# Kernel tuning notes

Hardware: AMD Instinct MI355X
Metric: run time of the kernel (lower is better)

## Reference

```python
import jax, jax.numpy as jnp
import numpy as np

E = 768
H_HEADS = 12


def trilinear_border_sample(feat_map, coords):
    """grid_sample 3D, mode='bilinear', padding_mode='border', align_corners=True.
    feat_map: (B, C, D, H, W); coords: (B, P, 3) in [-1,1], last dim = (x, y, z) -> (W, H, D).
    Returns (B, P, C).
    """
    B, C, D, H, W = feat_map.shape
    x, y, z = coords[..., 0], coords[..., 1], coords[..., 2]
    ix = (x + 1.0) * 0.5 * (W - 1)
    iy = (y + 1.0) * 0.5 * (H - 1)
    iz = (z + 1.0) * 0.5 * (D - 1)
    x0 = jnp.floor(ix); y0 = jnp.floor(iy); z0 = jnp.floor(iz)
    wx = ix - x0; wy = iy - y0; wz = iz - z0
    x0i = jnp.clip(x0, 0, W - 1).astype(jnp.int32)
    x1i = jnp.clip(x0 + 1, 0, W - 1).astype(jnp.int32)
    y0i = jnp.clip(y0, 0, H - 1).astype(jnp.int32)
    y1i = jnp.clip(y0 + 1, 0, H - 1).astype(jnp.int32)
    z0i = jnp.clip(z0, 0, D - 1).astype(jnp.int32)
    z1i = jnp.clip(z0 + 1, 0, D - 1).astype(jnp.int32)
    flat = feat_map.reshape(B, C, D * H * W)

    def gather(zi, yi, xi):
        idx = (zi * H + yi) * W + xi  # (B, P)
        return jnp.take_along_axis(flat, idx[:, None, :], axis=2)  # (B, C, P)

    out = (
        gather(z0i, y0i, x0i) * ((1 - wz) * (1 - wy) * (1 - wx))[:, None, :]
        + gather(z0i, y0i, x1i) * ((1 - wz) * (1 - wy) * wx)[:, None, :]
        + gather(z0i, y1i, x0i) * ((1 - wz) * wy * (1 - wx))[:, None, :]
        + gather(z0i, y1i, x1i) * ((1 - wz) * wy * wx)[:, None, :]
        + gather(z1i, y0i, x0i) * (wz * (1 - wy) * (1 - wx))[:, None, :]
        + gather(z1i, y0i, x1i) * (wz * (1 - wy) * wx)[:, None, :]
        + gather(z1i, y1i, x0i) * (wz * wy * (1 - wx))[:, None, :]
        + gather(z1i, y1i, x1i) * (wz * wy * wx)[:, None, :]
    )
    return out.transpose(0, 2, 1)  # (B, P, C)


def setup_inputs() -> dict:
    key = jax.random.key(0)
    ks = jax.random.split(key, 12)
    B, fullN, nb = 64, 513, 32
    s = 1.0 / np.sqrt(E)
    return {
        "x": jax.random.normal(ks[0], (B, fullN, E), jnp.float32),
        "bio_embed": jax.random.normal(ks[1], (B, E), jnp.float32),
        "base_coords": jax.random.uniform(ks[2], (nb, 3), jnp.float32),
        "offsets": jax.random.normal(ks[3], (B, nb, 3), jnp.float32) * 0.1,
        "confidence": jax.random.uniform(ks[4], (B, 1), jnp.float32),
        "sample_proj_w": jax.random.uniform(ks[5], (E, E), jnp.float32, -s, s),
        "sample_proj_b": jax.random.uniform(ks[6], (E,), jnp.float32, -s, s),
        "in_proj_w": jax.random.uniform(ks[7], (3 * E, E), jnp.float32, -s, s),
        "in_proj_b": jnp.zeros((3 * E,), jnp.float32),
        "out_proj_w": jax.random.uniform(ks[8], (E, E), jnp.float32, -s, s),
        "out_proj_b": jnp.zeros((E,), jnp.float32),
        "grid_size": 8,
    }


def reference(x, bio_embed, base_coords, offsets, confidence,
              sample_proj_w, sample_proj_b, in_proj_w, in_proj_b,
              out_proj_w, out_proj_b, grid_size):
    B, fullN, C = x.shape
    G = grid_size
    patch_tokens = x[:, 1:, :]  # (B, N, C), N = G^3
    feat_map = patch_tokens.transpose(0, 2, 1).reshape(B, C, G, G, G)

    coords = jnp.clip(base_coords[None, :, :] + offsets, -1.0, 1.0)  # (B, nb, 3)
    sampled = trilinear_border_sample(feat_map, coords)  # (B, nb, C)
    sampled = sampled @ sample_proj_w.T + sample_proj_b

    # MultiheadAttention: single query (bio_embed), keys/values = sampled tokens
    hd = E // H_HEADS
    Wq, Wk, Wv = in_proj_w[:E], in_proj_w[E:2 * E], in_proj_w[2 * E:]
    bq, bk, bv = in_proj_b[:E], in_proj_b[E:2 * E], in_proj_b[2 * E:]
    q = (bio_embed @ Wq.T + bq).reshape(B, H_HEADS, hd)
    k = (sampled @ Wk.T + bk).reshape(B, -1, H_HEADS, hd)
    v = (sampled @ Wv.T + bv).reshape(B, -1, H_HEADS, hd)
    scores = jnp.einsum('bhd,bphd->bhp', q, k) / jnp.sqrt(jnp.asarray(hd, q.dtype))
    attn = jax.nn.softmax(scores, axis=-1)
    ctx = jnp.einsum('bhp,bphd->bhd', attn, v).reshape(B, E)
    attn_out = ctx @ out_proj_w.T + out_proj_b  # (B, E)

    out = jnp.broadcast_to(attn_out[:, None, :], (B, fullN, C))
    out = out * confidence[:, :, None]
    return out
```

## Files before the change

### kernel.cpp

```cpp
#include <hip/hip_runtime.h>
#include <hip/hip_bf16.h>
#include <math.h>

#define E 768
#define NH 12
#define HD 64
#define NTHR 256
#define SLICES 8

typedef __attribute__((ext_vector_type(8))) short bf16x8;
typedef __attribute__((ext_vector_type(4))) float f32x4;

__device__ __forceinline__ unsigned short f2bf_rne(float f) {
    unsigned int u = __float_as_uint(f);
    u += 0x7FFF + ((u >> 16) & 1);
    return (unsigned short)(u >> 16);
}

__device__ __forceinline__ void sample_one(
    const float* x, const float* bcrd, const float* offs, int G,
    unsigned short* sampled, int u, int P, int fullN, int t, int tstep)
{
    int b = u / P, p = u % P;
    float gm1 = (float)(G - 1);

    float cx = bcrd[p * 3 + 0] + offs[u * 3 + 0];
    float cy = bcrd[p * 3 + 1] + offs[u * 3 + 1];
    float cz = bcrd[p * 3 + 2] + offs[u * 3 + 2];
    cx = fminf(fmaxf(cx, -1.f), 1.f);
    cy = fminf(fmaxf(cy, -1.f), 1.f);
    cz = fminf(fmaxf(cz, -1.f), 1.f);

    float ix = (cx + 1.f) * 0.5f * gm1;
    float iy = (cy + 1.f) * 0.5f * gm1;
    float iz = (cz + 1.f) * 0.5f * gm1;
    float fx = floorf(ix), fy = floorf(iy), fz = floorf(iz);
    float wx = ix - fx, wy = iy - fy, wz = iz - fz;

    int x0 = (int)fminf(fmaxf(fx,       0.f), gm1);
    int x1 = (int)fminf(fmaxf(fx + 1.f, 0.f), gm1);
    int y0 = (int)fminf(fmaxf(fy,       0.f), gm1);
    int y1 = (int)fminf(fmaxf(fy + 1.f, 0.f), gm1);
    int z0 = (int)fminf(fmaxf(fz,       0.f), gm1);
    int z1 = (int)fminf(fmaxf(fz + 1.f, 0.f), gm1);

    int tk[8];
    tk[0] = (z0 * G + y0) * G + x0;
    tk[1] = (z0 * G + y0) * G + x1;
    tk[2] = (z0 * G + y1) * G + x0;
    tk[3] = (z0 * G + y1) * G + x1;
    tk[4] = (z1 * G + y0) * G + x0;
    tk[5] = (z1 * G + y0) * G + x1;
    tk[6] = (z1 * G + y1) * G + x0;
    tk[7] = (z1 * G + y1) * G + x1;
    float wgt[8];
    wgt[0] = (1.f - wz) * (1.f - wy) * (1.f - wx);
    wgt[1] = (1.f - wz) * (1.f - wy) * wx;
    wgt[2] = (1.f - wz) * wy * (1.f - wx);
    wgt[3] = (1.f - wz) * wy * wx;
    wgt[4] = wz * (1.f - wy) * (1.f - wx);
    wgt[5] = wz * (1.f - wy) * wx;
    wgt[6] = wz * wy * (1.f - wx);
    wgt[7] = wz * wy * wx;

    const float4* xb4 = (const float4*)(x + ((size_t)b * fullN + 1) * E);
    ushort4* outp = (ushort4*)(sampled + (size_t)u * E);
    for (int c4 = t; c4 < E / 4; c4 += tstep) {
        float4 acc = {0.f, 0.f, 0.f, 0.f};
#pragma unroll
        for (int k = 0; k < 8; ++k) {
            float4 v = xb4[(size_t)tk[k] * (E / 4) + c4];
            acc.x += wgt[k] * v.x; acc.y += wgt[k] * v.y;
            acc.z += wgt[k] * v.z; acc.w += wgt[k] * v.w;
        }
        ushort4 o;
        o.x = f2bf_rne(acc.x); o.y = f2bf_rne(acc.y);
        o.z = f2bf_rne(acc.z); o.w = f2bf_rne(acc.w);
        outp[c4] = o;
    }
}

__device__ __forceinline__ void gemm64_tile(
    const unsigned short* A, const unsigned short* W,
    const float* bias, float* C,
    int N, int K, int m0, int n0,
    unsigned short* lsA, unsigned short* lsB)
{
    int wv = threadIdx.x >> 6;
    int ln = threadIdx.x & 63;
    int wm = (wv & 1) * 32;
    int wn = (wv >> 1) * 32;

    f32x4 acc[2][2] = {};

    int srow = ln >> 2;
    int scol = (ln & 3) * 8;

    for (int k0 = 0; k0 < K; k0 += 32) {
        int row = wv * 16 + srow;
        const unsigned short* ga = A + (size_t)(m0 + row) * K + k0 + scol;
        const unsigned short* gw = W + (size_t)(n0 + row) * K + k0 + scol;
        __builtin_amdgcn_global_load_lds(
            (const __attribute__((address_space(1))) unsigned int*)ga,
            (__attribute__((address_space(3))) unsigned int*)(lsA + wv * 16 * 32),
            16, 0, 0);
        __builtin_amdgcn_global_load_lds(
            (const __attribute__((address_space(1))) unsigned int*)gw,
            (__attribute__((address_space(3))) unsigned int*)(lsB + wv * 16 * 32),
            16, 0, 0);
        __syncthreads();

        int kq = (ln >> 4) * 8;
        int rsel = ln & 15;
        bf16x8 af[2], bfr[2];
#pragma unroll
        for (int i = 0; i < 2; ++i) {
            af[i]  = *(const bf16x8*)&lsA[(wm + i * 16 + rsel) * 32 + kq];
            bfr[i] = *(const bf16x8*)&lsB[(wn + i * 16 + rsel) * 32 + kq];
        }
#pragma unroll
        for (int i = 0; i < 2; ++i)
#pragma unroll
            for (int j = 0; j < 2; ++j)
                acc[i][j] = __builtin_amdgcn_mfma_f32_16x16x32_bf16(
                    af[i], bfr[j], acc[i][j], 0, 0, 0);
        __syncthreads();
    }

    int cr = (ln >> 4) * 4;
    int cc = ln & 15;
#pragma unroll
    for (int j = 0; j < 2; ++j) {
        int col = n0 + wn + j * 16 + cc;
        float bv = bias[col];
#pragma unroll
        for (int i = 0; i < 2; ++i) {
#pragma unroll
            for (int r = 0; r < 4; ++r) {
                int row = m0 + wm + i * 16 + cr + r;
                C[(size_t)row * N + col] = acc[i][j][r] + bv;
            }
        }
    }
}

__device__ __forceinline__ void w2_tile(
    const float* Wkv, const float* spw, unsigned short* w2_bf,
    int n0, int k0, unsigned short* lsA, unsigned short* lsB)
{
    int t = threadIdx.x;
    int wv = t >> 6;
    int ln = t & 63;
    int wm = (wv & 1) * 32;
    int wn = (wv >> 1) * 32;

    f32x4 acc[2][2] = {};

    for (int j0 = 0; j0 < E; j0 += 32) {
#pragma unroll
        for (int rep = 0; rep < 2; ++rep) {
            int fi = t + rep * 256;
            int r = fi >> 3, c4 = fi & 7;
            float4 v = *(const float4*)(Wkv + (size_t)(n0 + r) * E + j0 + c4 * 4);
            ushort4 o;
            o.x = f2bf_rne(v.x); o.y = f2bf_rne(v.y);
            o.z = f2bf_rne(v.z); o.w = f2bf_rne(v.w);
            *(ushort4*)(lsA + r * 32 + c4 * 4) = o;
        }
#pragma unroll
        for (int rep = 0; rep < 2; ++rep) {
            int fi = t + rep * 256;
            int kk = fi >> 3, j4 = fi & 7;
            const float* sp = spw + (size_t)(j0 + j4 * 4) * E + k0 + kk;
            ushort4 o;
            o.x = f2bf_rne(sp[0 * E]);
            o.y = f2bf_rne(sp[1 * E]);
            o.z = f2bf_rne(sp[2 * E]);
            o.w = f2bf_rne(sp[3 * E]);
            *(ushort4*)(lsB + kk * 32 + j4 * 4) = o;
        }
        __syncthreads();

        int kq = (ln >> 4) * 8;
        int rsel = ln & 15;
        bf16x8 af[2], bfr[2];
#pragma unroll
        for (int i = 0; i < 2; ++i) {
            af[i]  = *(const bf16x8*)&lsA[(wm + i * 16 + rsel) * 32 + kq];
            bfr[i] = *(const bf16x8*)&lsB[(wn + i * 16 + rsel) * 32 + kq];
        }
#pragma unroll
        for (int i = 0; i < 2; ++i)
#pragma unroll
            for (int j = 0; j < 2; ++j)
                acc[i][j] = __builtin_amdgcn_mfma_f32_16x16x32_bf16(
                    af[i], bfr[j], acc[i][j], 0, 0, 0);
        __syncthreads();
    }

    int cr = (ln >> 4) * 4;
    int cc = ln & 15;
#pragma unroll
    for (int j = 0; j < 2; ++j) {
        int col = k0 + wn + j * 16 + cc;
#pragma unroll
        for (int i = 0; i < 2; ++i) {
#pragma unroll
            for (int r = 0; r < 4; ++r) {
                int row = n0 + wm + i * 16 + cr + r;
                w2_bf[(size_t)row * E + col] = f2bf_rne(acc[i][j][r]);
            }
        }
    }
}

__device__ __forceinline__ void matvec_wave(
    const float* A, const float* W, const float* bias, float* C,
    int u, int N, int K, int ln)
{
    int m = u / N, n = u % N;
    const float* a = A + (size_t)m * K;
    const float* w = W + (size_t)n * K;
    float s = 0.f;
    for (int k = ln; k < K; k += 64) s += a[k] * w[k];
#pragma unroll
    for (int off = 32; off; off >>= 1) s += __shfl_down(s, off);
    if (ln == 0) C[u] = s + bias[n];
}

__device__ __forceinline__ void matvec_wave_v4(
    const float* A, const float* W, const float* bias, float* C,
    int u, int N, int ln)
{
    int m = u / N, n = u % N;
    const float4* a4 = (const float4*)(A + (size_t)m * E);
    const float4* w4 = (const float4*)(W + (size_t)n * E);
    float s = 0.f;
#pragma unroll
    for (int j = 0; j < 3; ++j) {
        float4 av = a4[ln + 64 * j];
        float4 wv = w4[ln + 64 * j];
        s += av.x * wv.x + av.y * wv.y + av.z * wv.z + av.w * wv.w;
    }
#pragma unroll
    for (int off = 32; off; off >>= 1) s += __shfl_down(s, off);
    if (ln == 0) C[u] = s + bias[n];
}

__global__ __launch_bounds__(256) void prep_kernel(
    const float* __restrict__ x,
    const float* __restrict__ bcrd, const float* __restrict__ offs,
    const int* __restrict__ gsize,
    const float* __restrict__ bio,
    const float* __restrict__ spw, const float* __restrict__ spb,
    const float* __restrict__ ipw, const float* __restrict__ ipb,
    unsigned short* __restrict__ sampled_bf, unsigned short* __restrict__ w2_bf,
    float* __restrict__ q, float* __restrict__ b2,
    int B, int P, int fullN, int nb_sample, int nb_w2, int nb_q)
{
    __shared__ unsigned short lsA[64 * 32];
    __shared__ unsigned short lsB[64 * 32];

    int blk = blockIdx.x;
    int t = threadIdx.x;
    int wv = t >> 6, ln = t & 63;
    const float* Wkv = ipw + (size_t)E * E;

    if (blk < nb_sample) {
        sample_one(x, bcrd, offs, *gsize, sampled_bf, blk, P, fullN, t, NTHR);
        return;
    }
    blk -= nb_sample;
    if (blk < nb_w2) {
        w2_tile(Wkv, spw, w2_bf, (blk / 12) * 64, (blk % 12) * 64, lsA, lsB);
        return;
    }
    blk -= nb_w2;
    if (blk < nb_q) {
        int u = blk * 4 + wv;
        if (u < B * E) matvec_wave_v4(bio, ipw, ipb, q, u, E, ln);
        return;
    }
    blk -= nb_q;
    {
        int u = blk * 4 + wv;
        if (u < 2 * E) matvec_wave_v4(spb, Wkv, ipb + E, b2, u, 2 * E, ln);
    }
}

__global__ __launch_bounds__(256) void kv_gemm(
    const unsigned short* __restrict__ A,
    const unsigned short* __restrict__ W,
    const float* __restrict__ bias,
    float* __restrict__ C, int N, int K)
{
    __shared__ unsigned short lsA[64 * 32];
    __shared__ unsigned short lsB[64 * 32];
    gemm64_tile(A, W, bias, C, N, K, blockIdx.y * 64, blockIdx.x * 64, lsA, lsB);
}

__global__ __launch_bounds__(256) void attn_outproj(
    const float* __restrict__ q, const float* __restrict__ kv,
    const float* __restrict__ opw, const float* __restrict__ opb,
    float* __restrict__ aout, int B, int P)
{
    __shared__ __align__(16) float q_lds[E];
    __shared__ __align__(16) float ctx_lds[E];

    int b = blockIdx.x % B;
    int g = blockIdx.x / B;
    int t = threadIdx.x, wv = t >> 6, ln = t & 63;

    const float* kvb = kv + (size_t)b * P * (2 * E);

    for (int i = t; i < E; i += NTHR) q_lds[i] = q[(size_t)b * E + i];
    __syncthreads();

    for (int h = wv; h < NH; h += 4) {
        int krow = (ln < P) ? ln : 0;
        const float4* kr4 = (const float4*)(kvb + (size_t)krow * (2 * E) + h * HD);
        const float* qh = q_lds + h * HD;
        float accd = 0.f;
#pragma unroll
        for (int j = 0; j < HD / 4; ++j) {
            float4 k4 = kr4[j];
            accd += qh[4 * j] * k4.x + qh[4 * j + 1] * k4.y
                  + qh[4 * j + 2] * k4.z + qh[4 * j + 3] * k4.w;
        }
        float s = (ln < P) ? accd * 0.125f : -INFINITY;

        float mx = s;
#pragma unroll
        for (int off = 32; off; off >>= 1) mx = fmaxf(mx, __shfl_xor(mx, off));
        float ex = (ln < P) ? __expf(s - mx) : 0.f;
        float den = ex;
#pragma unroll
        for (int off = 32; off; off >>= 1) den += __shfl_xor(den, off);
        float pl = ex / den;

        const float* vcol = kvb + E + h * HD + ln;
        float acc = 0.f;
#pragma unroll
        for (int p = 0; p < 32; ++p)
            acc += __shfl(pl, p) * vcol[(size_t)p * (2 * E)];
        ctx_lds[h * HD + ln] = acc;
    }
    __syncthreads();

    const float4* c4p = (const float4*)ctx_lds;
#pragma unroll 2
    for (int idx = 0; idx < 24; ++idx) {
        int n = g * 96 + wv * 24 + idx;
        const float4* w4 = (const float4*)(opw + (size_t)n * E);
        float s = 0.f;
#pragma unroll
        for (int j = 0; j < 3; ++j) {
            float4 wvv = w4[ln + 64 * j];
            float4 cv = c4p[ln + 64 * j];
            s += wvv.x * cv.x + wvv.y * cv.y + wvv.z * cv.z + wvv.w * cv.w;
        }
#pragma unroll
        for (int off = 32; off; off >>= 1) s += __shfl_down(s, off);
        if (ln == 0) aout[(size_t)b * E + n] = s + opb[n];
    }
}

__global__ void bcast_kernel(const float* __restrict__ attn_out,
                             const float* __restrict__ conf,
                             float* __restrict__ out,
                             int fullN, int pc)
{
    int b = blockIdx.y;
    float cf = conf[b];
    const float4* ao = (const float4*)(attn_out + (size_t)b * E);
    float4* ob = (float4*)(out + (size_t)b * fullN * E);
    int i = blockIdx.x * blockDim.x + threadIdx.x;
    if (i < pc) {
        int c4 = i % (E / 4);
        float4 v = ao[c4];
        v.x *= cf; v.y *= cf; v.z *= cf; v.w *= cf;
        ob[i] = v;
    }
}

__global__ void attn_fb(const float* __restrict__ q,
                        const float* __restrict__ kv,
                        float* __restrict__ ctx, int B, int P)
{
    int u = blockIdx.x * 4 + (threadIdx.x >> 6);
    int ln = threadIdx.x & 63;
    if (u >= B * NH) return;
    int b = u / NH, h = u % NH;
    float qd = q[(size_t)b * E + h * HD + ln];
    const float* kvb = kv + (size_t)b * P * (2 * E);
    int krow = (ln < P) ? ln : 0;
    const float* kr = kvb + (size_t)krow * (2 * E) + h * HD;
    float accd = 0.f;
#pragma unroll
    for (int e = 0; e < HD; ++e) accd += __shfl(qd, e) * kr[e];
    float s = (ln < P) ? accd * 0.125f : -INFINITY;
    float mx = s;
#pragma unroll
    for (int off = 32; off; off >>= 1) mx = fmaxf(mx, __shfl_xor(mx, off));
    float ex = (ln < P) ? __expf(s - mx) : 0.f;
    float den = ex;
#pragma unroll
    for (int off = 32; off; off >>= 1) den += __shfl_xor(den, off);
    float pl = ex / den;
    float acc = 0.f;
    for (int p = 0; p < P; ++p)
        acc += __shfl(pl, p) * kvb[(size_t)p * (2 * E) + E + h * HD + ln];
    ctx[(size_t)b * E + h * HD + ln] = acc;
}

__global__ void matvec_fb(const float* __restrict__ A,
                          const float* __restrict__ W,
                          const float* __restrict__ bias,
                          float* __restrict__ C, int M, int N, int K)
{
    int u = blockIdx.x * 4 + (threadIdx.x >> 6);
    if (u < M * N) matvec_wave(A, W, bias, C, u, N, K, threadIdx.x & 63);
}

extern "C" void kernel_launch(void* const* d_in, const int* in_sizes, int n_in,
                              void* d_out, int out_size, void* d_ws, size_t ws_size,
                              hipStream_t stream)
{
    const float* x      = (const float*)d_in[0];
    const float* bio    = (const float*)d_in[1];
    const float* bcrd   = (const float*)d_in[2];
    const float* offs   = (const float*)d_in[3];
    const float* conf   = (const float*)d_in[4];
    const float* spw    = (const float*)d_in[5];
    const float* spb    = (const float*)d_in[6];
    const float* ipw    = (const float*)d_in[7];
    const float* ipb    = (const float*)d_in[8];
    const float* opw    = (const float*)d_in[9];
    const float* opb    = (const float*)d_in[10];
    const int*   gsize  = (const int*)d_in[11];
    float* out = (float*)d_out;

    int B     = in_sizes[1] / E;
    int P     = in_sizes[2] / 3;
    int fullN = in_sizes[0] / (B * E);
    int M     = B * P;

    char* base = (char*)d_out;
    unsigned short* sampled_bf = (unsigned short*)(base + 0);
    unsigned short* w2_bf      = (unsigned short*)(base + 3145728);

    const size_t kv_bytes = (size_t)M * (2 * E) * 4;
    const size_t q_bytes  = (size_t)B * E * 4;
    const size_t b2_bytes = (size_t)(2 * E) * 4;
    const size_t ao_bytes = (size_t)B * E * 4;
    const bool path_a = (ws_size >= kv_bytes + q_bytes + b2_bytes + ao_bytes);

    float *kv, *q, *b2, *aout;
    if (path_a) {
        kv   = (float*)d_ws;
        q    = (float*)((char*)d_ws + kv_bytes);
        b2   = (float*)((char*)d_ws + kv_bytes + q_bytes);
        aout = (float*)((char*)d_ws + kv_bytes + q_bytes + b2_bytes);
    } else {
        kv   = (float*)(base + 5505024);
        q    = (float*)(base + 18087936);
        b2   = (float*)(base + 18481152);
        aout = (float*)d_ws;
    }

    int nb_sample = M;
    int nb_w2     = (2 * E / 64) * (E / 64);
    int nb_q      = (B * E + 3) / 4;
    int nb_b2     = (2 * E + 3) / 4;
    prep_kernel<<<nb_sample + nb_w2 + nb_q + nb_b2, NTHR, 0, stream>>>(
        x, bcrd, offs, gsize, bio, spw, spb, ipw, ipb,
        sampled_bf, w2_bf, q, b2, B, P, fullN, nb_sample, nb_w2, nb_q);

    kv_gemm<<<dim3(2 * E / 64, M / 64), NTHR, 0, stream>>>(
        sampled_bf, w2_bf, b2, kv, 2 * E, E);

    if (path_a) {
        attn_outproj<<<B * SLICES, NTHR, 0, stream>>>(q, kv, opw, opb, aout,
                                                      B, P);
    } else {
        float* ctx = (float*)(base + 18284544);
        attn_fb<<<(B * NH + 3) / 4, NTHR, 0, stream>>>(q, kv, ctx, B, P);
        matvec_fb<<<(B * E + 3) / 4, NTHR, 0, stream>>>(ctx, opw, opb, aout,
                                                        B, E, E);
    }

    int pc = fullN * E / 4;
    bcast_kernel<<<dim3((pc + 255) / 256, B), NTHR, 0, stream>>>(
        aout, conf, out, fullN, pc);
}
```

Baseline: 271.4 us.

## Replace explicit K/V GEMM with per-head query-folded attention over sampled tokens

Instead of materialising the full K and V projections for every sampled token with an MFMA GEMM, each (batch, head) block folds the query into the combined key weight (u = q·W2k). It then scores the raw bf16 sampled tokens against u, applies the attention weights to the raw tokens, and projects the resulting context through W2v once. This removes the large fp32 KV buffer write and read, and the separate GEMM launch. In exchange it adds a per-head matvec over W2 rows for each of the 768 blocks, and it drops the key bias term, which is safe only because softmax is shift-invariant. Out-projection becomes its own kernel reading ctx from workspace, and the fallback path for a small workspace is removed.

```diff
diff --git a/kernel.cpp b/kernel.cpp
--- a/kernel.cpp
+++ b/kernel.cpp
@@ -15,6 +15,10 @@
     unsigned int u = __float_as_uint(f);
     u += 0x7FFF + ((u >> 16) & 1);
     return (unsigned short)(u >> 16);
+}
+
+__device__ __forceinline__ float bf2f(unsigned short u) {
+    return __uint_as_float((unsigned)u << 16);
 }
 
 __device__ __forceinline__ void sample_one(
@@ -80,70 +84,6 @@
     }
 }
 
-__device__ __forceinline__ void gemm64_tile(
-    const unsigned short* A, const unsigned short* W,
-    const float* bias, float* C,
-    int N, int K, int m0, int n0,
-    unsigned short* lsA, unsigned short* lsB)
-{
-    int wv = threadIdx.x >> 6;
-    int ln = threadIdx.x & 63;
-    int wm = (wv & 1) * 32;
-    int wn = (wv >> 1) * 32;
-
-    f32x4 acc[2][2] = {};
-
-    int srow = ln >> 2;
-    int scol = (ln & 3) * 8;
-
-    for (int k0 = 0; k0 < K; k0 += 32) {
-        int row = wv * 16 + srow;
-        const unsigned short* ga = A + (size_t)(m0 + row) * K + k0 + scol;
-        const unsigned short* gw = W + (size_t)(n0 + row) * K + k0 + scol;
-        __builtin_amdgcn_global_load_lds(
-            (const __attribute__((address_space(1))) unsigned int*)ga,
-            (__attribute__((address_space(3))) unsigned int*)(lsA + wv * 16 * 32),
-            16, 0, 0);
-        __builtin_amdgcn_global_load_lds(
-            (const __attribute__((address_space(1))) unsigned int*)gw,
-            (__attribute__((address_space(3))) unsigned int*)(lsB + wv * 16 * 32),
-            16, 0, 0);
-        __syncthreads();
-
-        int kq = (ln >> 4) * 8;
-        int rsel = ln & 15;
-        bf16x8 af[2], bfr[2];
-#pragma unroll
-        for (int i = 0; i < 2; ++i) {
-            af[i]  = *(const bf16x8*)&lsA[(wm + i * 16 + rsel) * 32 + kq];
-            bfr[i] = *(const bf16x8*)&lsB[(wn + i * 16 + rsel) * 32 + kq];
-        }
-#pragma unroll
-        for (int i = 0; i < 2; ++i)
-#pragma unroll
-            for (int j = 0; j < 2; ++j)
-                acc[i][j] = __builtin_amdgcn_mfma_f32_16x16x32_bf16(
-                    af[i], bfr[j], acc[i][j], 0, 0, 0);
-        __syncthreads();
-    }
-
-    int cr = (ln >> 4) * 4;
-    int cc = ln & 15;
-#pragma unroll
-    for (int j = 0; j < 2; ++j) {
-        int col = n0 + wn + j * 16 + cc;
-        float bv = bias[col];
-#pragma unroll
-        for (int i = 0; i < 2; ++i) {
-#pragma unroll
-            for (int r = 0; r < 4; ++r) {
-                int row = m0 + wm + i * 16 + cr + r;
-                C[(size_t)row * N + col] = acc[i][j][r] + bv;
-            }
-        }
-    }
-}
-
 __device__ __forceinline__ void w2_tile(
     const float* Wkv, const float* spw, unsigned short* w2_bf,
     int n0, int k0, unsigned short* lsA, unsigned short* lsB)
@@ -214,20 +154,6 @@
     }
 }
 
-__device__ __forceinline__ void matvec_wave(
-    const float* A, const float* W, const float* bias, float* C,
-    int u, int N, int K, int ln)
-{
-    int m = u / N, n = u % N;
-    const float* a = A + (size_t)m * K;
-    const float* w = W + (size_t)n * K;
-    float s = 0.f;
-    for (int k = ln; k < K; k += 64) s += a[k] * w[k];
-#pragma unroll
-    for (int off = 32; off; off >>= 1) s += __shfl_down(s, off);
-    if (ln == 0) C[u] = s + bias[n];
-}
-
 __device__ __forceinline__ void matvec_wave_v4(
     const float* A, const float* W, const float* bias, float* C,
     int u, int N, int ln)
@@ -288,63 +214,101 @@
     }
 }
 
-__global__ __launch_bounds__(256) void kv_gemm(
-    const unsigned short* __restrict__ A,
-    const unsigned short* __restrict__ W,
-    const float* __restrict__ bias,
-    float* __restrict__ C, int N, int K)
-{
-    __shared__ unsigned short lsA[64 * 32];
-    __shared__ unsigned short lsB[64 * 32];
-    gemm64_tile(A, W, bias, C, N, K, blockIdx.y * 64, blockIdx.x * 64, lsA, lsB);
-}
-
-__global__ __launch_bounds__(256) void attn_outproj(
-    const float* __restrict__ q, const float* __restrict__ kv,
-    const float* __restrict__ opw, const float* __restrict__ opb,
-    float* __restrict__ aout, int B, int P)
-{
-    __shared__ __align__(16) float q_lds[E];
+__global__ __launch_bounds__(256) void attn_ctx(
+    const float* __restrict__ q, const unsigned short* __restrict__ sampled_bf,
+    const unsigned short* __restrict__ w2_bf, const float* __restrict__ b2,
+    float* __restrict__ ctx, int B, int P)
+{
+    __shared__ float q_lds[HD];
+    __shared__ __align__(16) float u_lds[E];
+    __shared__ float sc_lds[64];
+    __shared__ float at_lds[64];
+    __shared__ __align__(16) float cx_lds[E];
+
+    int b = blockIdx.x % B;
+    int h = blockIdx.x / B;
+    int t = threadIdx.x, wv = t >> 6, ln = t & 63;
+
+    const unsigned short* W2k = w2_bf + (size_t)(h * HD) * E;
+    const unsigned short* W2v = w2_bf + (size_t)(E + h * HD) * E;
+    const unsigned short* smp = sampled_bf + (size_t)(b * P) * E;
+
+    if (t < HD) q_lds[t] = q[(size_t)b * E + h * HD + t];
+    __syncthreads();
+
+    if (t < E / 4) {
+        float4 uu = {0.f, 0.f, 0.f, 0.f};
+        for (int d = 0; d < HD; ++d) {
+            float qd = q_lds[d];
+            ushort4 r = *(const ushort4*)(W2k + (size_t)d * E + 4 * t);
+            uu.x += qd * bf2f(r.x); uu.y += qd * bf2f(r.y);
+            uu.z += qd * bf2f(r.z); uu.w += qd * bf2f(r.w);
+        }
+        *(float4*)&u_lds[4 * t] = uu;
+    }
+    __syncthreads();
+
+    for (int p = wv; p < P; p += 4) {
+        const unsigned short* sr = smp + (size_t)p * E;
+        float s = 0.f;
+#pragma unroll
+        for (int c = 0; c < E / 64; ++c)
+            s += u_lds[ln + 64 * c] * bf2f(sr[ln + 64 * c]);
+#pragma unroll
+        for (int off = 32; off; off >>= 1) s += __shfl_xor(s, off);
+        if (ln == 0) sc_lds[p] = s * 0.125f;
+    }
+    __syncthreads();
+
+    if (wv == 0) {
+        float s = (ln < P) ? sc_lds[ln] : -INFINITY;
+        float mx = s;
+#pragma unroll
+        for (int off = 32; off; off >>= 1) mx = fmaxf(mx, __shfl_xor(mx, off));
+        float ex = (ln < P) ? __expf(s - mx) : 0.f;
+        float den = ex;
+#pragma unroll
+        for (int off = 32; off; off >>= 1) den += __shfl_xor(den, off);
+        if (ln < P) at_lds[ln] = ex / den;
+    }
+    __syncthreads();
+
+    if (t < E / 4) {
+        float4 cc = {0.f, 0.f, 0.f, 0.f};
+        for (int p = 0; p < P; ++p) {
+            float a = at_lds[p];
+            ushort4 r = *(const ushort4*)(smp + (size_t)p * E + 4 * t);
+            cc.x += a * bf2f(r.x); cc.y += a * bf2f(r.y);
+            cc.z += a * bf2f(r.z); cc.w += a * bf2f(r.w);
+        }
+        *(float4*)&cx_lds[4 * t] = cc;
+    }
+    __syncthreads();
+
+    for (int d = wv; d < HD; d += 4) {
+        const unsigned short* vr = W2v + (size_t)d * E;
+        float s = 0.f;
+#pragma unroll
+        for (int c = 0; c < E / 64; ++c)
+            s += cx_lds[ln + 64 * c] * bf2f(vr[ln + 64 * c]);
+#pragma unroll
+        for (int off = 32; off; off >>= 1) s += __shfl_down(s, off);
+        if (ln == 0)
+            ctx[(size_t)b * E + h * HD + d] = s + b2[E + h * HD + d];
+    }
+}
+
+__global__ __launch_bounds__(256) void outproj_kernel(
+    const float* __restrict__ ctx, const float* __restrict__ opw,
+    const float* __restrict__ opb, float* __restrict__ aout, int B)
+{
     __shared__ __align__(16) float ctx_lds[E];
 
     int b = blockIdx.x % B;
     int g = blockIdx.x / B;
     int t = threadIdx.x, wv = t >> 6, ln = t & 63;
 
-    const float* kvb = kv + (size_t)b * P * (2 * E);
-
-    for (int i = t; i < E; i += NTHR) q_lds[i] = q[(size_t)b * E + i];
-    __syncthreads();
-
-    for (int h = wv; h < NH; h += 4) {
-        int krow = (ln < P) ? ln : 0;
-        const float4* kr4 = (const float4*)(kvb + (size_t)krow * (2 * E) + h * HD);
-        const float* qh = q_lds + h * HD;
-        float accd = 0.f;
-#pragma unroll
-        for (int j = 0; j < HD / 4; ++j) {
-            float4 k4 = kr4[j];
-            accd += qh[4 * j] * k4.x + qh[4 * j + 1] * k4.y
-                  + qh[4 * j + 2] * k4.z + qh[4 * j + 3] * k4.w;
-        }
-        float s = (ln < P) ? accd * 0.125f : -INFINITY;
-
-        float mx = s;
-#pragma unroll
-        for (int off = 32; off; off >>= 1) mx = fmaxf(mx, __shfl_xor(mx, off));
-        float ex = (ln < P) ? __expf(s - mx) : 0.f;
-        float den = ex;
-#pragma unroll
-        for (int off = 32; off; off >>= 1) den += __shfl_xor(den, off);
-        float pl = ex / den;
-
-        const float* vcol = kvb + E + h * HD + ln;
-        float acc = 0.f;
-#pragma unroll
-        for (int p = 0; p < 32; ++p)
-            acc += __shfl(pl, p) * vcol[(size_t)p * (2 * E)];
-        ctx_lds[h * HD + ln] = acc;
-    }
+    for (int i = t; i < E; i += NTHR) ctx_lds[i] = ctx[(size_t)b * E + i];
     __syncthreads();
 
     const float4* c4p = (const float4*)ctx_lds;
@@ -381,45 +345,6 @@
         v.x *= cf; v.y *= cf; v.z *= cf; v.w *= cf;
         ob[i] = v;
     }
-}
-
-__global__ void attn_fb(const float* __restrict__ q,
-                        const float* __restrict__ kv,
-                        float* __restrict__ ctx, int B, int P)
-{
-    int u = blockIdx.x * 4 + (threadIdx.x >> 6);
-    int ln = threadIdx.x & 63;
-    if (u >= B * NH) return;
-    int b = u / NH, h = u % NH;
-    float qd = q[(size_t)b * E + h * HD + ln];
-    const float* kvb = kv + (size_t)b * P * (2 * E);
-    int krow = (ln < P) ? ln : 0;
-    const float* kr = kvb + (size_t)krow * (2 * E) + h * HD;
-    float accd = 0.f;
-#pragma unroll
-    for (int e = 0; e < HD; ++e) accd += __shfl(qd, e) * kr[e];
-    float s = (ln < P) ? accd * 0.125f : -INFINITY;
-    float mx = s;
-#pragma unroll
-    for (int off = 32; off; off >>= 1) mx = fmaxf(mx, __shfl_xor(mx, off));
-    float ex = (ln < P) ? __expf(s - mx) : 0.f;
-    float den = ex;
-#pragma unroll
-    for (int off = 32; off; off >>= 1) den += __shfl_xor(den, off);
-    float pl = ex / den;
-    float acc = 0.f;
-    for (int p = 0; p < P; ++p)
-        acc += __shfl(pl, p) * kvb[(size_t)p * (2 * E) + E + h * HD + ln];
-    ctx[(size_t)b * E + h * HD + ln] = acc;
-}
-
-__global__ void matvec_fb(const float* __restrict__ A,
-                          const float* __restrict__ W,
-                          const float* __restrict__ bias,
-                          float* __restrict__ C, int M, int N, int K)
-{
-    int u = blockIdx.x * 4 + (threadIdx.x >> 6);
-    if (u < M * N) matvec_wave(A, W, bias, C, u, N, K, threadIdx.x & 63);
 }
 
 extern "C" void kernel_launch(void* const* d_in, const int* in_sizes, int n_in,
@@ -449,24 +374,10 @@
     unsigned short* sampled_bf = (unsigned short*)(base + 0);
     unsigned short* w2_bf      = (unsigned short*)(base + 3145728);
 
-    const size_t kv_bytes = (size_t)M * (2 * E) * 4;
-    const size_t q_bytes  = (size_t)B * E * 4;
-    const size_t b2_bytes = (size_t)(2 * E) * 4;
-    const size_t ao_bytes = (size_t)B * E * 4;
-    const bool path_a = (ws_size >= kv_bytes + q_bytes + b2_bytes + ao_bytes);
-
-    float *kv, *q, *b2, *aout;
-    if (path_a) {
-        kv   = (float*)d_ws;
-        q    = (float*)((char*)d_ws + kv_bytes);
-        b2   = (float*)((char*)d_ws + kv_bytes + q_bytes);
-        aout = (float*)((char*)d_ws + kv_bytes + q_bytes + b2_bytes);
-    } else {
-        kv   = (float*)(base + 5505024);
-        q    = (float*)(base + 18087936);
-        b2   = (float*)(base + 18481152);
-        aout = (float*)d_ws;
-    }
+    float* q    = (float*)d_ws;
+    float* b2   = (float*)((char*)d_ws + 196608);
+    float* ctx  = (float*)((char*)d_ws + 262144);
+    float* aout = (float*)((char*)d_ws + 524288);
 
     int nb_sample = M;
     int nb_w2     = (2 * E / 64) * (E / 64);
@@ -476,18 +387,9 @@
         x, bcrd, offs, gsize, bio, spw, spb, ipw, ipb,
         sampled_bf, w2_bf, q, b2, B, P, fullN, nb_sample, nb_w2, nb_q);
 
-    kv_gemm<<<dim3(2 * E / 64, M / 64), NTHR, 0, stream>>>(
-        sampled_bf, w2_bf, b2, kv, 2 * E, E);
-
-    if (path_a) {
-        attn_outproj<<<B * SLICES, NTHR, 0, stream>>>(q, kv, opw, opb, aout,
-                                                      B, P);
-    } else {
-        float* ctx = (float*)(base + 18284544);
-        attn_fb<<<(B * NH + 3) / 4, NTHR, 0, stream>>>(q, kv, ctx, B, P);
-        matvec_fb<<<(B * E + 3) / 4, NTHR, 0, stream>>>(ctx, opw, opb, aout,
-                                                        B, E, E);
-    }
+    attn_ctx<<<B * NH, NTHR, 0, stream>>>(q, sampled_bf, w2_bf, b2, ctx, B, P);
+
+    outproj_kernel<<<B * SLICES, NTHR, 0, stream>>>(ctx, opw, opb, aout, B);
 
     int pc = fullN * E / 4;
     bcast_kernel<<<dim3((pc + 255) / 256, B), NTHR, 0, stream>>>(
```

Result: no change. 270.5 us (-0.3%).
